# Performance work log

Measured on AMD Instinct MI355X. Metric: run time of the kernel, lower is better.

## Reference

```python
import jax, jax.numpy as jnp
import numpy as np

N, D_IN, D_HID, D_OUT, E = 8192, 1024, 4096, 1024, 8
N_ACTIVE = max(1, int(E * 0.625))  # 5
TEMP = float(np.e)               # temperature = np.e in source


def setup_inputs() -> dict:
    key = jax.random.key(0)
    ks = jax.random.split(key, 4)
    return {
        "x": jax.random.normal(ks[0], (N, D_IN), jnp.float32),
        "gate_w": jax.random.normal(ks[1], (D_IN, E), jnp.float32) * 0.02,
        "gate_b": jnp.zeros((E,), jnp.float32),
        "w1": jax.random.normal(ks[2], (E, D_IN, D_HID), jnp.float32) * 0.02,
        "b1": jnp.zeros((E, D_HID), jnp.float32),
        "w2": jax.random.normal(ks[3], (E, D_HID, D_OUT), jnp.float32) * 0.02,
        "b2": jnp.zeros((E, D_OUT), jnp.float32),
    }


def reference(x, gate_w, gate_b, w1, b1, w2, b2):
    # Gate: softmax over experts at temperature e, then top-k mask + renormalize
    scores = (x @ gate_w + gate_b) / TEMP                 # [N, E]
    probs = jax.nn.softmax(scores, axis=-1)               # [N, E]
    _, topk_idx = jax.lax.top_k(probs, N_ACTIVE)          # [N, k]
    mask = jax.nn.one_hot(topk_idx, E, dtype=probs.dtype).sum(axis=-2)  # [N, E]
    weights = probs * mask
    weights = weights / (weights.sum(axis=-1, keepdims=True) + 1e-8)
    # Dense all-experts FFN (dropout is eval-mode identity)
    h = jax.nn.relu(jnp.einsum('nd,edh->neh', x, w1) + b1)   # [N, E, d_hid]
    e_out = jnp.einsum('neh,eho->neo', h, w2) + b2           # [N, E, d_out]
    # Camp A (first E/2 experts) added, camp G subtracted: out = out_a - out_g
    sign = jnp.where(jnp.arange(E) < E // 2, 1.0, -1.0)      # [E]
    return jnp.einsum('ne,neo->no', weights * sign, e_out)   # [N, d_out]
```

## Files before the change

kernel.cpp:

```cpp
#include <hip/hip_runtime.h>
#include <hip/hip_bf16.h>
#include <cmath>


typedef _Float16 f16;
typedef _Float16 f16x8 __attribute__((ext_vector_type(8)));
typedef _Float16 f16x4 __attribute__((ext_vector_type(4)));
typedef float f32x4 __attribute__((ext_vector_type(4)));

#define NROWS 8192
#define DIN   1024
#define DHID  4096
#define DOUT  1024
#define NEXP  8

#define OFF_SGATE 0u
#define OFF_XH    262144u
#define OFF_W1T   17039360u
#define OFF_W2T   84148224u
#define OFF_HHS   151257088u
#define OFF_P1    218365952u
#define NEED_MID  251920384ull

__device__ __forceinline__ void gload_lds16(const void* gsrc, void* ldsdst) {
  __builtin_amdgcn_global_load_lds(
      (const __attribute__((address_space(1))) unsigned int*)gsrc,
      (__attribute__((address_space(3))) unsigned int*)ldsdst, 16, 0, 0);
}

__global__ void gate_kernel(const float* __restrict__ x,
                            const float* __restrict__ gw,
                            const float* __restrict__ gb,
                            float* __restrict__ sgate) {
  const int row = blockIdx.x * 4 + (threadIdx.x >> 6);
  const int l = threadIdx.x & 63;
  const float* xr = x + (size_t)row * DIN;
  float acc[8] = {0.f,0.f,0.f,0.f,0.f,0.f,0.f,0.f};
#pragma unroll
  for (int j = 0; j < 16; ++j) {
    const int k = l + 64 * j;
    const float xv = xr[k];
    const float4 g0 = *(const float4*)(gw + (size_t)k * 8);
    const float4 g1 = *(const float4*)(gw + (size_t)k * 8 + 4);
    acc[0] += xv * g0.x; acc[1] += xv * g0.y; acc[2] += xv * g0.z; acc[3] += xv * g0.w;
    acc[4] += xv * g1.x; acc[5] += xv * g1.y; acc[6] += xv * g1.z; acc[7] += xv * g1.w;
  }
#pragma unroll
  for (int off = 32; off > 0; off >>= 1) {
#pragma unroll
    for (int e = 0; e < 8; ++e) acc[e] += __shfl_xor(acc[e], off, 64);
  }
  if (l == 0) {
    const float invT = 0.36787944117144233f;
    float p[8]; float mx = -1e30f;
#pragma unroll
    for (int e = 0; e < 8; ++e) { p[e] = (acc[e] + gb[e]) * invT; mx = fmaxf(mx, p[e]); }
    float S = 0.f;
#pragma unroll
    for (int e = 0; e < 8; ++e) { p[e] = expf(p[e] - mx); S += p[e]; }
    const float inv = 1.0f / S;
#pragma unroll
    for (int e = 0; e < 8; ++e) p[e] *= inv;
    bool keep[8] = {true,true,true,true,true,true,true,true};
    for (int t = 0; t < 3; ++t) {
      float pmin = 1e30f; int mi = -1;
      for (int e = 0; e < 8; ++e)
        if (keep[e] && (p[e] < pmin || (p[e] == pmin && e > mi))) { pmin = p[e]; mi = e; }
      keep[mi] = false;
    }
    float wsum = 0.f;
#pragma unroll
    for (int e = 0; e < 8; ++e) if (keep[e]) wsum += p[e];
    const float rinv = 1.0f / (wsum + 1e-8f);
#pragma unroll
    for (int e = 0; e < 8; ++e) {
      const float wv = keep[e] ? p[e] * rinv : 0.0f;
      sgate[(size_t)row * 8 + e] = (e < 4) ? wv : -wv;
    }
  }
}

__global__ void cvt_x_kernel(const float* __restrict__ x, f16* __restrict__ xh) {
  const size_t i = ((size_t)blockIdx.x * blockDim.x + threadIdx.x) * 4;
  const float4 v = *(const float4*)(x + i);
  f16x4 o = { (f16)v.x, (f16)v.y, (f16)v.z, (f16)v.w };
  *(f16x4*)(xh + i) = o;
}

__global__ void transpose_cvt(const float* __restrict__ in, f16* __restrict__ out,
                              int R, int C) {
  __shared__ float tile[32][33];
  const int e = blockIdx.z;
  const float* ine = in + (size_t)e * R * C;
  f16* oute = out + (size_t)e * R * C;
  const int c0 = blockIdx.x * 32, r0 = blockIdx.y * 32;
  const int tx = threadIdx.x, ty = threadIdx.y;
#pragma unroll
  for (int i = 0; i < 4; ++i)
    tile[ty + i * 8][tx] = ine[(size_t)(r0 + ty + i * 8) * C + c0 + tx];
  __syncthreads();
#pragma unroll
  for (int i = 0; i < 4; ++i)
    oute[(size_t)(c0 + ty + i * 8) * R + r0 + tx] = (f16)tile[tx][ty + i * 8];
}

#define MFMAOP(a_, b_, c_) __builtin_amdgcn_mfma_f32_16x16x32_f16(a_, b_, c_, 0, 0, 0)

template <int EPI>
__global__ __launch_bounds__(512, 2) void gemm8p(
    const f16* __restrict__ A, int lda,
    const f16* __restrict__ B, int ldb, int nt,
    const float* __restrict__ bias,
    f16* __restrict__ outH, int ldc,
    float* outP0, float* outP1, int p1w,
    const float* __restrict__ sgate, int expert, int gx) {
  __shared__ alignas(16) f16 lA[4 * 8192];
  __shared__ alignas(16) f16 lB[4 * 8192];
  const int tid = threadIdx.x;
  const int l = tid & 63, w = tid >> 6;
  const int wr = w >> 2, wc = w & 3;

  const int nwg = gridDim.x, cpx = nwg >> 3;
  const int lg = ((int)blockIdx.x & 7) * cpx + ((int)blockIdx.x >> 3);

  int m0, n0;
  const f16* Aeff = A;
  const f16* Beff = B;
  float* P = nullptr;
  bool pw = false;
  if constexpr (EPI == 1) {
    m0 = (lg / gx) * 256; n0 = (lg % gx) * 256;
  } else {
    const int xx = lg >> 5, cc = lg & 31;
    const int kh = xx >> 2;
    n0 = (xx & 3) * 256;
    m0 = cc * 256;
    Aeff = A + kh * 2048;
    Beff = B + kh * 2048;
    P = kh ? outP1 : outP0;
    pw = (p1w != 0);
  }

  const int srow = tid >> 3;
  const int sxc = (tid & 7) ^ (srow & 7);
  const f16* pA = Aeff + (size_t)(m0 + srow) * lda + sxc * 8;
  const f16* pB = Beff + (size_t)(n0 + srow) * ldb + sxc * 8;
  f16* const dA = lA + w * 512;
  f16* const dB = lB + w * 512;

#define STG_A(slot, h, tk) do { \
    const f16* s_ = pA + (size_t)(h) * 128 * lda + (size_t)(tk) * 64; \
    gload_lds16(s_,            dA + (slot) * 8192); \
    gload_lds16(s_ + 64 * lda, dA + (slot) * 8192 + 4096); \
  } while (0)
#define STG_B(slot, h, tk) do { \
    const f16* s_ = pB + (size_t)(h) * 128 * ldb + (size_t)(tk) * 64; \
    gload_lds16(s_,            dB + (slot) * 8192); \
    gload_lds16(s_ + 64 * ldb, dB + (slot) * 8192 + 4096); \
  } while (0)

  const int cg = l >> 4, xr = l & 7;
  const int ok0 = ((cg ^ xr) << 4);
  const int ok1 = (((4 + cg) ^ xr) << 4);
  const char* const baA = (const char*)lA + (l & 15) * 128;
  const char* const baB = (const char*)lB + (wc & 1) * 8192 + (l & 15) * 128;

#define RDA(CA, f, o) (*(const f16x8*)(baA + ((CA) + wr) * 16384 + (f) * 2048 + (o)))
#define RDB(CB, g, o) (*(const f16x8*)(baB + ((CB) + (wc >> 1)) * 16384 + (g) * 2048 + (o)))
#define SYNC() do { __builtin_amdgcn_s_barrier(); \
    asm volatile("s_waitcnt lgkmcnt(0)" ::: "memory"); \
    __builtin_amdgcn_sched_barrier(0); } while (0)
#define ENDPH() do { __builtin_amdgcn_s_setprio(0); \
    __builtin_amdgcn_s_barrier(); } while (0)
#define VM6() do { asm volatile("s_waitcnt vmcnt(6)" ::: "memory"); \
    __builtin_amdgcn_sched_barrier(0); } while (0)
#define MM(f, g, ar, br) acc[f][g] = MFMAOP(ar, br, acc[f][g])

  f32x4 acc[8][4] = {};
  f16x8 aA0,aA1,aB0,aB1,aC0,aC1,aD0,aD1;
  f16x8 b00,b01,b10,b11,b20,b21,b30,b31;

#define TILEBODY(T, CA, CB, SB1, SB0n, SA0n, SA1n) do { \
     \
    aA0 = RDA(CA, 0, ok0); aA1 = RDA(CA, 0, ok1); \
    aB0 = RDA(CA, 1, ok0); aB1 = RDA(CA, 1, ok1); \
    aC0 = RDA(CA, 2, ok0); aC1 = RDA(CA, 2, ok1); \
    aD0 = RDA(CA, 3, ok0); aD1 = RDA(CA, 3, ok1); \
    b00 = RDB(CB, 0, ok0); b01 = RDB(CB, 0, ok1); \
    b10 = RDB(CB, 1, ok0); b11 = RDB(CB, 1, ok1); \
    if ((T) + 1 < nt) STG_B(SB1, 1, (T) + 1); \
    SYNC(); \
    __builtin_amdgcn_s_setprio(1); \
    MM(0,0,aA0,b00); MM(0,1,aA0,b10); MM(1,0,aB0,b00); MM(1,1,aB0,b10); \
    MM(2,0,aC0,b00); MM(2,1,aC0,b10); MM(3,0,aD0,b00); MM(3,1,aD0,b10); \
    MM(0,0,aA1,b01); MM(0,1,aA1,b11); MM(1,0,aB1,b01); MM(1,1,aB1,b11); \
    MM(2,0,aC1,b01); MM(2,1,aC1,b11); MM(3,0,aD1,b01); MM(3,1,aD1,b11); \
    ENDPH(); \
     \
    b20 = RDB(CB, 2, ok0); b21 = RDB(CB, 2, ok1); \
    b30 = RDB(CB, 3, ok0); b31 = RDB(CB, 3, ok1); \
    SYNC(); \
    __builtin_amdgcn_s_setprio(1); \
    MM(0,2,aA0,b20); MM(0,3,aA0,b30); MM(1,2,aB0,b20); MM(1,3,aB0,b30); \
    MM(2,2,aC0,b20); MM(2,3,aC0,b30); MM(3,2,aD0,b20); MM(3,3,aD0,b30); \
    MM(0,2,aA1,b21); MM(0,3,aA1,b31); MM(1,2,aB1,b21); MM(1,3,aB1,b31); \
    MM(2,2,aC1,b21); MM(2,3,aC1,b31); MM(3,2,aD1,b21); MM(3,3,aD1,b31); \
    ENDPH(); \
     \
    aA0 = RDA(CA, 4, ok0); aA1 = RDA(CA, 4, ok1); \
    aB0 = RDA(CA, 5, ok0); aB1 = RDA(CA, 5, ok1); \
    aC0 = RDA(CA, 6, ok0); aC1 = RDA(CA, 6, ok1); \
    aD0 = RDA(CA, 7, ok0); aD1 = RDA(CA, 7, ok1); \
    if ((T) + 2 < nt) STG_B(SB0n, 0, (T) + 2); \
    SYNC(); \
    __builtin_amdgcn_s_setprio(1); \
    MM(4,0,aA0,b00); MM(4,1,aA0,b10); MM(5,0,aB0,b00); MM(5,1,aB0,b10); \
    MM(6,0,aC0,b00); MM(6,1,aC0,b10); MM(7,0,aD0,b00); MM(7,1,aD0,b10); \
    MM(4,0,aA1,b01); MM(4,1,aA1,b11); MM(5,0,aB1,b01); MM(5,1,aB1,b11); \
    MM(6,0,aC1,b01); MM(6,1,aC1,b11); MM(7,0,aD1,b01); MM(7,1,aD1,b11); \
    ENDPH(); \
     \
    if ((T) + 2 < nt) { STG_A(SA0n, 0, (T) + 2); STG_A(SA1n, 1, (T) + 2); } \
    VM6(); \
    SYNC(); \
    __builtin_amdgcn_s_setprio(1); \
    MM(4,2,aA0,b20); MM(4,3,aA0,b30); MM(5,2,aB0,b20); MM(5,3,aB0,b30); \
    MM(6,2,aC0,b20); MM(6,3,aC0,b30); MM(7,2,aD0,b20); MM(7,3,aD0,b30); \
    MM(4,2,aA1,b21); MM(4,3,aA1,b31); MM(5,2,aB1,b21); MM(5,3,aB1,b31); \
    MM(6,2,aC1,b21); MM(6,3,aC1,b31); MM(7,2,aD1,b21); MM(7,3,aD1,b31); \
    ENDPH(); \
  } while (0)

  STG_A(0, 0, 0); STG_B(0, 0, 0); STG_A(1, 1, 0); STG_B(1, 1, 0);
  STG_A(2, 0, 1); STG_B(2, 0, 1); STG_A(3, 1, 1);
  asm volatile("s_waitcnt vmcnt(6)" ::: "memory");
  __builtin_amdgcn_s_barrier();

  for (int t = 0; t < nt; t += 2) {
    TILEBODY(t,     0, 0, 3, 0, 0, 1);
    TILEBODY(t + 1, 2, 2, 1, 2, 2, 3);
  }
  asm volatile("s_waitcnt vmcnt(0)" ::: "memory");

  if constexpr (EPI == 1) {
#pragma unroll
    for (int mi = 0; mi < 8; ++mi)
#pragma unroll
      for (int r = 0; r < 4; ++r) {
        const int row = m0 + wr * 128 + mi * 16 + (l >> 4) * 4 + r;
        const float sg = sgate[(size_t)row * 8 + expert];
#pragma unroll
        for (int ni = 0; ni < 4; ++ni) {
          const int col = n0 + wc * 64 + ni * 16 + (l & 15);
          const float v = acc[mi][ni][r] + bias[col];
          outH[(size_t)row * ldc + col] = (f16)(fmaxf(v, 0.0f) * sg);
        }
      }
  } else {
    float* const scr = (w < 4) ? (float*)lA + w * 4096
                               : (float*)lB + (w - 4) * 4096;
    const int hl = l >> 4, ll = l & 15;
#pragma unroll
    for (int p = 0; p < 2; ++p) {
#pragma unroll
      for (int mi4 = 0; mi4 < 4; ++mi4)
#pragma unroll
        for (int r = 0; r < 4; ++r) {
          const int rowl = mi4 * 16 + hl * 4 + r;
#pragma unroll
          for (int ni = 0; ni < 4; ++ni)
            scr[rowl * 64 + ni * 16 + ll] = acc[p * 4 + mi4][ni][r];
        }
#pragma unroll
      for (int i = 0; i < 16; ++i) {
        const int rowl = hl + i * 4;
        f32x4 v = *(const f32x4*)(scr + rowl * 64 + ll * 4);
        const int row = m0 + wr * 128 + p * 64 + rowl;
        const int col = n0 + wc * 64 + ll * 4;
        f32x4* gp = (f32x4*)(P + (size_t)row * 1024 + col);
        if (!pw) {
          const f32x4 g = *gp;
          v[0] += g[0]; v[1] += g[1]; v[2] += g[2]; v[3] += g[3];
        }
        *gp = v;
      }
    }
  }
#undef STG_A
#undef STG_B
#undef RDA
#undef RDB
#undef SYNC
#undef ENDPH
#undef VM6
#undef MM
#undef TILEBODY
}

template <bool WITHP>
__global__ void finalize_out(const float* p0,
                             const float* __restrict__ p1,
                             const float* __restrict__ sgate,
                             const float* __restrict__ b2,
                             float* out) {
  const int i = blockIdx.x * 256 + threadIdx.x;
  const int n = i >> 8, c4 = i & 255;
  float4 a = make_float4(0.f, 0.f, 0.f, 0.f);
  if constexpr (WITHP) {
    const float4 u = ((const float4*)p0)[i];
    const float4 v = ((const float4*)p1)[i];
    a.x = u.x + v.x; a.y = u.y + v.y; a.z = u.z + v.z; a.w = u.w + v.w;
  }
  const float* sg = sgate + (size_t)n * 8;
#pragma unroll
  for (int e = 0; e < 8; ++e) {
    const float s = sg[e];
    const float4 bv = ((const float4*)(b2 + (size_t)e * 1024))[c4];
    a.x += s * bv.x; a.y += s * bv.y; a.z += s * bv.z; a.w += s * bv.w;
  }
  ((float4*)out)[i] = a;
}

__global__ __launch_bounds__(512, 2) void gemm_acc(
    const f16* __restrict__ A, const f16* __restrict__ Bt,
    float* __restrict__ Out, int N, int K, int gx) {
  __shared__ alignas(16) f16 lA[3 * 256 * 64];
  __shared__ alignas(16) f16 lB[3 * 128 * 64];
  const int tid = threadIdx.x;
  const int l = tid & 63, w = tid >> 6;
  const int wr = w >> 1, wc = w & 1;
  const int nwg = gridDim.x, cpx = nwg >> 3;
  const int lg = ((int)blockIdx.x & 7) * cpx + ((int)blockIdx.x >> 3);
  const int bx = lg % gx, by = lg / gx;
  const int m0 = by * 256, n0 = bx * 128;

  const int srow = tid >> 3;
  const int scol = (((tid & 7) ^ (srow & 7)) << 3);
  const f16* Ab = A + ((size_t)m0 + srow) * K + scol;
  const f16* Bb = Bt + ((size_t)n0 + srow) * K + scol;
  f16* const dA = &lA[w * 512];
  f16* const dB = &lB[w * 512];

  int aoff[4][2], boff[4][2];
#pragma unroll
  for (int f = 0; f < 4; ++f) {
    const int ar = wr * 64 + f * 16 + (l & 15);
    const int br = wc * 64 + f * 16 + (l & 15);
#pragma unroll
    for (int ks = 0; ks < 2; ++ks) {
      const int cb = ks * 64 + ((l >> 4) << 4);
      aoff[f][ks] = ar * 64 + ((cb ^ ((ar & 7) << 4)) >> 1);
      boff[f][ks] = br * 64 + ((cb ^ ((br & 7) << 4)) >> 1);
    }
  }
  f32x4 acc[4][4] = {};
  f16x8 b[4][2];
  f16x8 aA, aB, aC, aD;
#define STAGE_A(bs, t) do { \
    const f16* s_ = Ab + (size_t)(t) * 64; \
    gload_lds16(s_,                   dA + (bs) * 16384); \
    gload_lds16(s_ + (size_t)64 * K,  dA + (bs) * 16384 + 4096); \
    gload_lds16(s_ + (size_t)128 * K, dA + (bs) * 16384 + 8192); \
    gload_lds16(s_ + (size_t)192 * K, dA + (bs) * 16384 + 12288); \
  } while (0)
#define STAGE_B(bs, t) do { \
    const f16* s_ = Bb + (size_t)(t) * 64; \
    gload_lds16(s_,                   dB + (bs) * 8192); \
    gload_lds16(s_ + (size_t)64 * K,  dB + (bs) * 8192 + 4096); \
  } while (0)
#define LOAD_B(bs) do { \
    b[0][0] = *(const f16x8*)&lB[(bs) * 8192 + boff[0][0]]; \
    b[0][1] = *(const f16x8*)&lB[(bs) * 8192 + boff[0][1]]; \
    b[1][0] = *(const f16x8*)&lB[(bs) * 8192 + boff[1][0]]; \
    b[1][1] = *(const f16x8*)&lB[(bs) * 8192 + boff[1][1]]; \
    b[2][0] = *(const f16x8*)&lB[(bs) * 8192 + boff[2][0]]; \
    b[2][1] = *(const f16x8*)&lB[(bs) * 8192 + boff[2][1]]; \
    b[3][0] = *(const f16x8*)&lB[(bs) * 8192 + boff[3][0]]; \
    b[3][1] = *(const f16x8*)&lB[(bs) * 8192 + boff[3][1]]; \
  } while (0)
#define LOAD_A4(bs, m0_, m1_) do { \
    aA = *(const f16x8*)&lA[(bs) * 16384 + aoff[m0_][0]]; \
    aB = *(const f16x8*)&lA[(bs) * 16384 + aoff[m0_][1]]; \
    aC = *(const f16x8*)&lA[(bs) * 16384 + aoff[m1_][0]]; \
    aD = *(const f16x8*)&lA[(bs) * 16384 + aoff[m1_][1]]; \
  } while (0)
#define CLUSTER(m0_, m1_) do { \
    __builtin_amdgcn_s_setprio(1); \
    acc[m0_][0] = MFMAOP(aA, b[0][0], acc[m0_][0]); \
    acc[m0_][1] = MFMAOP(aA, b[1][0], acc[m0_][1]); \
    acc[m0_][2] = MFMAOP(aA, b[2][0], acc[m0_][2]); \
    acc[m0_][3] = MFMAOP(aA, b[3][0], acc[m0_][3]); \
    acc[m1_][0] = MFMAOP(aC, b[0][0], acc[m1_][0]); \
    acc[m1_][1] = MFMAOP(aC, b[1][0], acc[m1_][1]); \
    acc[m1_][2] = MFMAOP(aC, b[2][0], acc[m1_][2]); \
    acc[m1_][3] = MFMAOP(aC, b[3][0], acc[m1_][3]); \
    acc[m0_][0] = MFMAOP(aB, b[0][1], acc[m0_][0]); \
    acc[m0_][1] = MFMAOP(aB, b[1][1], acc[m0_][1]); \
    acc[m0_][2] = MFMAOP(aB, b[2][1], acc[m0_][2]); \
    acc[m0_][3] = MFMAOP(aB, b[3][1], acc[m0_][3]); \
    acc[m1_][0] = MFMAOP(aD, b[0][1], acc[m1_][0]); \
    acc[m1_][1] = MFMAOP(aD, b[1][1], acc[m1_][1]); \
    acc[m1_][2] = MFMAOP(aD, b[2][1], acc[m1_][2]); \
    acc[m1_][3] = MFMAOP(aD, b[3][1], acc[m1_][3]); \
    __builtin_amdgcn_s_setprio(0); \
  } while (0)
#define BAR() asm volatile("s_barrier" ::: "memory")
#define VMC6() asm volatile("s_waitcnt vmcnt(6)" ::: "memory")
  const int niter = K >> 7, ntiles = K >> 6;
  STAGE_A(0, 0); STAGE_B(0, 0);
  STAGE_A(1, 1); STAGE_B(1, 1);
  VMC6();
  BAR();
  int bp = 0, bq = 1, brr = 2;
  int t2 = 2, t3 = 3;
  for (int i = 0; i < niter; ++i) {
    LOAD_B(bp); LOAD_A4(bp, 0, 1);
    STAGE_A(brr, t2);
    BAR(); CLUSTER(0, 1); BAR();
    LOAD_A4(bp, 2, 3);
    STAGE_B(brr, t2);
    VMC6(); BAR(); CLUSTER(2, 3); BAR();
    LOAD_B(bq); LOAD_A4(bq, 0, 1);
    STAGE_A(bp, t3);
    BAR(); CLUSTER(0, 1); BAR();
    LOAD_A4(bq, 2, 3);
    STAGE_B(bp, t3);
    VMC6(); BAR(); CLUSTER(2, 3); BAR();
    const int tmp = bp; bp = brr; brr = bq; bq = tmp;
    t2 += 2; if (t2 >= ntiles) t2 -= ntiles;
    t3 += 2; if (t3 >= ntiles) t3 -= ntiles;
  }
  asm volatile("s_waitcnt vmcnt(0)" ::: "memory");
#pragma unroll
  for (int mi = 0; mi < 4; ++mi)
#pragma unroll
    for (int r = 0; r < 4; ++r) {
      const int row = m0 + wr * 64 + mi * 16 + (l >> 4) * 4 + r;
#pragma unroll
      for (int ni = 0; ni < 4; ++ni) {
        const int col = n0 + wc * 64 + ni * 16 + (l & 15);
        Out[(size_t)row * N + col] += acc[mi][ni][r];
      }
    }
#undef STAGE_A
#undef STAGE_B
#undef LOAD_B
#undef LOAD_A4
#undef CLUSTER
#undef BAR
#undef VMC6
}

extern "C" void kernel_launch(void* const* d_in, const int* in_sizes, int n_in,
                              void* d_out, int out_size, void* d_ws, size_t ws_size,
                              hipStream_t stream) {
  const float* x  = (const float*)d_in[0];
  const float* gw = (const float*)d_in[1];
  const float* gb = (const float*)d_in[2];
  const float* w1 = (const float*)d_in[3];
  const float* b1 = (const float*)d_in[4];
  const float* w2 = (const float*)d_in[5];
  const float* b2 = (const float*)d_in[6];
  float* out = (float*)d_out;

  char* ws = (char*)d_ws;
  float* sgate = (float*)(ws + OFF_SGATE);
  f16* xh  = (f16*)(ws + OFF_XH);
  f16* w1t = (f16*)(ws + OFF_W1T);
  f16* w2t = (f16*)(ws + OFF_W2T);
  f16* hhs = (f16*)(ws + OFF_HHS);
  float* p1 = (float*)(ws + OFF_P1);

  const bool mid = (ws_size >= NEED_MID);

  gate_kernel<<<NROWS / 4, 256, 0, stream>>>(x, gw, gb, sgate);
  cvt_x_kernel<<<(NROWS * DIN) / (256 * 4), 256, 0, stream>>>(x, xh);
  transpose_cvt<<<dim3(DHID / 32, DIN / 32, NEXP), dim3(32, 8), 0, stream>>>(w1, w1t, DIN, DHID);
  transpose_cvt<<<dim3(DOUT / 32, DHID / 32, NEXP), dim3(32, 8), 0, stream>>>(w2, w2t, DHID, DOUT);

  if (mid) {
    for (int e = 0; e < NEXP; ++e) {
      gemm8p<1><<<512, 512, 0, stream>>>(
          xh, DIN, w1t + (size_t)e * DHID * DIN, DIN, DIN / 64,
          b1 + (size_t)e * DHID, hhs, DHID,
          nullptr, nullptr, 0, sgate, e, DHID / 256);
      gemm8p<2><<<256, 512, 0, stream>>>(
          hhs, DHID, w2t + (size_t)e * DOUT * DHID, DHID, 2048 / 64,
          nullptr, nullptr, 0, out, p1, (e == 0) ? 1 : 0, nullptr, 0, DOUT / 256);
    }
    finalize_out<true><<<(NROWS * DOUT) / (256 * 4), 256, 0, stream>>>(
        out, p1, sgate, b2, out);
  } else {
    finalize_out<false><<<(NROWS * DOUT) / (256 * 4), 256, 0, stream>>>(
        nullptr, nullptr, sgate, b2, out);
    for (int e = 0; e < NEXP; ++e) {
      gemm8p<1><<<512, 512, 0, stream>>>(
          xh, DIN, w1t + (size_t)e * DHID * DIN, DIN, DIN / 64,
          b1 + (size_t)e * DHID, hhs, DHID,
          nullptr, nullptr, 0, sgate, e, DHID / 256);
      gemm_acc<<<256, 512, 0, stream>>>(hhs, w2t + (size_t)e * DOUT * DHID,
                                        out, DOUT, DHID, DOUT / 128);
    }
  }
}
```

Before: 1.545 ms.

## Batch experts into grouped second GEMM with K=32 four-stage LDS pipeline

The GEMM tile loop changes from a K=64 step with three staged slots to a K=32 step with a four-slot ring and a new swizzle. The host now writes hidden activations for up to 8 experts side by side in a wider buffer, sized to fit the workspace. A single second GEMM then runs over the concatenated K of all experts in the group, so the fp32 partial sums are read and written once per group instead of once per expert. The fallback gemm_acc path is removed, and the workspace offsets and requirements change to match.

```diff
diff --git a/kernel.cpp b/kernel.cpp
--- a/kernel.cpp
+++ b/kernel.cpp
@@ -18,9 +18,12 @@
 #define OFF_XH    262144u
 #define OFF_W1T   17039360u
 #define OFF_W2T   84148224u
-#define OFF_HHS   151257088u
-#define OFF_P1    218365952u
-#define NEED_MID  251920384ull
+#define OFF_P1    151257088u
+#define OFF_HH    184811520u
+#define NEED_NE1  251920384ull
+#define NEED_NE2  319029248ull
+#define NEED_NE4  453246976ull
+#define NEED_NE8  721682432ull
 
 __device__ __forceinline__ void gload_lds16(const void* gsrc, void* ldsdst) {
   __builtin_amdgcn_global_load_lds(
@@ -110,6 +113,7 @@
 __global__ __launch_bounds__(512, 2) void gemm8p(
     const f16* __restrict__ A, int lda,
     const f16* __restrict__ B, int ldb, int nt,
+    long long khA, long long khB,
     const float* __restrict__ bias,
     f16* __restrict__ outH, int ldc,
     float* outP0, float* outP1, int p1w,
@@ -135,110 +139,100 @@
     const int kh = xx >> 2;
     n0 = (xx & 3) * 256;
     m0 = cc * 256;
-    Aeff = A + kh * 2048;
-    Beff = B + kh * 2048;
+    Aeff = A + (size_t)kh * (size_t)khA;
+    Beff = B + (size_t)kh * (size_t)khB;
     P = kh ? outP1 : outP0;
     pw = (p1w != 0);
   }
 
-  const int srow = tid >> 3;
-  const int sxc = (tid & 7) ^ (srow & 7);
+  const int srow = tid >> 2;
+  const int sxc = (tid & 3) ^ ((tid >> 3) & 3);
   const f16* pA = Aeff + (size_t)(m0 + srow) * lda + sxc * 8;
   const f16* pB = Beff + (size_t)(n0 + srow) * ldb + sxc * 8;
-  f16* const dA = lA + w * 512;
-  f16* const dB = lB + w * 512;
-
-#define STG_A(slot, h, tk) do { \
-    const f16* s_ = pA + (size_t)(h) * 128 * lda + (size_t)(tk) * 64; \
-    gload_lds16(s_,            dA + (slot) * 8192); \
-    gload_lds16(s_ + 64 * lda, dA + (slot) * 8192 + 4096); \
-  } while (0)
-#define STG_B(slot, h, tk) do { \
-    const f16* s_ = pB + (size_t)(h) * 128 * ldb + (size_t)(tk) * 64; \
-    gload_lds16(s_,            dB + (slot) * 8192); \
-    gload_lds16(s_ + 64 * ldb, dB + (slot) * 8192 + 4096); \
-  } while (0)
-
-  const int cg = l >> 4, xr = l & 7;
-  const int ok0 = ((cg ^ xr) << 4);
-  const int ok1 = (((4 + cg) ^ xr) << 4);
-  const char* const baA = (const char*)lA + (l & 15) * 128;
-  const char* const baB = (const char*)lB + (wc & 1) * 8192 + (l & 15) * 128;
-
-#define RDA(CA, f, o) (*(const f16x8*)(baA + ((CA) + wr) * 16384 + (f) * 2048 + (o)))
-#define RDB(CB, g, o) (*(const f16x8*)(baB + ((CB) + (wc >> 1)) * 16384 + (g) * 2048 + (o)))
+
+  auto BOFS = [&](int tk) -> size_t {
+    if constexpr (EPI == 1) return (size_t)tk * 32;
+    else return (size_t)(tk >> 7) * (size_t)(DOUT * DHID) +
+                (size_t)(tk & 127) * 32;
+  };
+
+#define STG_A(S, H, TK) \
+    gload_lds16(pA + (size_t)(H) * 128 * lda + (size_t)(TK) * 32, \
+                lA + (S) * 8192 + (H) * 4096 + w * 512)
+#define STG_B(S, H, TK) \
+    gload_lds16(pB + (size_t)(H) * 128 * ldb + BOFS(TK), \
+                lB + (S) * 8192 + (H) * 4096 + w * 512)
+
+  int aofs[8], bofs4[4];
+  {
+    const int cg = l >> 4;
+#pragma unroll
+    for (int f = 0; f < 8; ++f) {
+      const int r = wr * 128 + f * 16 + (l & 15);
+      aofs[f] = r * 64 + ((cg ^ ((r >> 1) & 3)) << 4);
+    }
+#pragma unroll
+    for (int g = 0; g < 4; ++g) {
+      const int r = wc * 64 + g * 16 + (l & 15);
+      bofs4[g] = r * 64 + ((cg ^ ((r >> 1) & 3)) << 4);
+    }
+  }
+#define RA(S, f) (*(const f16x8*)((const char*)lA + (S) * 16384 + aofs[f]))
+#define RB(S, g) (*(const f16x8*)((const char*)lB + (S) * 16384 + bofs4[g]))
+
 #define SYNC() do { __builtin_amdgcn_s_barrier(); \
     asm volatile("s_waitcnt lgkmcnt(0)" ::: "memory"); \
     __builtin_amdgcn_sched_barrier(0); } while (0)
 #define ENDPH() do { __builtin_amdgcn_s_setprio(0); \
     __builtin_amdgcn_s_barrier(); } while (0)
-#define VM6() do { asm volatile("s_waitcnt vmcnt(6)" ::: "memory"); \
+#define VM8() do { asm volatile("s_waitcnt vmcnt(8)" ::: "memory"); \
+    __builtin_amdgcn_sched_barrier(0); } while (0)
+#define VM4() do { asm volatile("s_waitcnt vmcnt(4)" ::: "memory"); \
+    __builtin_amdgcn_sched_barrier(0); } while (0)
+#define VM0() do { asm volatile("s_waitcnt vmcnt(0)" ::: "memory"); \
     __builtin_amdgcn_sched_barrier(0); } while (0)
 #define MM(f, g, ar, br) acc[f][g] = MFMAOP(ar, br, acc[f][g])
 
   f32x4 acc[8][4] = {};
-  f16x8 aA0,aA1,aB0,aB1,aC0,aC1,aD0,aD1;
-  f16x8 b00,b01,b10,b11,b20,b21,b30,b31;
-
-#define TILEBODY(T, CA, CB, SB1, SB0n, SA0n, SA1n) do { \
+  f16x8 fa0, fa1, fa2, fa3;
+  f16x8 fb0, fb1, fb2, fb3;
+
+#define BODY(T, S, S3) do { \
      \
-    aA0 = RDA(CA, 0, ok0); aA1 = RDA(CA, 0, ok1); \
-    aB0 = RDA(CA, 1, ok0); aB1 = RDA(CA, 1, ok1); \
-    aC0 = RDA(CA, 2, ok0); aC1 = RDA(CA, 2, ok1); \
-    aD0 = RDA(CA, 3, ok0); aD1 = RDA(CA, 3, ok1); \
-    b00 = RDB(CB, 0, ok0); b01 = RDB(CB, 0, ok1); \
-    b10 = RDB(CB, 1, ok0); b11 = RDB(CB, 1, ok1); \
-    if ((T) + 1 < nt) STG_B(SB1, 1, (T) + 1); \
+    fa0 = RA(S, 0); fa1 = RA(S, 1); fa2 = RA(S, 2); fa3 = RA(S, 3); \
+    fb0 = RB(S, 0); fb1 = RB(S, 1); fb2 = RB(S, 2); fb3 = RB(S, 3); \
+    if ((T) + 3 < nt) { STG_A(S3, 0, (T) + 3); STG_A(S3, 1, (T) + 3); } \
     SYNC(); \
     __builtin_amdgcn_s_setprio(1); \
-    MM(0,0,aA0,b00); MM(0,1,aA0,b10); MM(1,0,aB0,b00); MM(1,1,aB0,b10); \
-    MM(2,0,aC0,b00); MM(2,1,aC0,b10); MM(3,0,aD0,b00); MM(3,1,aD0,b10); \
-    MM(0,0,aA1,b01); MM(0,1,aA1,b11); MM(1,0,aB1,b01); MM(1,1,aB1,b11); \
-    MM(2,0,aC1,b01); MM(2,1,aC1,b11); MM(3,0,aD1,b01); MM(3,1,aD1,b11); \
+    MM(0,0,fa0,fb0); MM(0,1,fa0,fb1); MM(0,2,fa0,fb2); MM(0,3,fa0,fb3); \
+    MM(1,0,fa1,fb0); MM(1,1,fa1,fb1); MM(1,2,fa1,fb2); MM(1,3,fa1,fb3); \
+    MM(2,0,fa2,fb0); MM(2,1,fa2,fb1); MM(2,2,fa2,fb2); MM(2,3,fa2,fb3); \
+    MM(3,0,fa3,fb0); MM(3,1,fa3,fb1); MM(3,2,fa3,fb2); MM(3,3,fa3,fb3); \
     ENDPH(); \
      \
-    b20 = RDB(CB, 2, ok0); b21 = RDB(CB, 2, ok1); \
-    b30 = RDB(CB, 3, ok0); b31 = RDB(CB, 3, ok1); \
+    fa0 = RA(S, 4); fa1 = RA(S, 5); fa2 = RA(S, 6); fa3 = RA(S, 7); \
+    if ((T) + 3 < nt) { STG_B(S3, 0, (T) + 3); STG_B(S3, 1, (T) + 3); } \
+    if ((T) + 3 < nt) VM8(); else if ((T) + 2 < nt) VM4(); else VM0(); \
     SYNC(); \
     __builtin_amdgcn_s_setprio(1); \
-    MM(0,2,aA0,b20); MM(0,3,aA0,b30); MM(1,2,aB0,b20); MM(1,3,aB0,b30); \
-    MM(2,2,aC0,b20); MM(2,3,aC0,b30); MM(3,2,aD0,b20); MM(3,3,aD0,b30); \
-    MM(0,2,aA1,b21); MM(0,3,aA1,b31); MM(1,2,aB1,b21); MM(1,3,aB1,b31); \
-    MM(2,2,aC1,b21); MM(2,3,aC1,b31); MM(3,2,aD1,b21); MM(3,3,aD1,b31); \
-    ENDPH(); \
-     \
-    aA0 = RDA(CA, 4, ok0); aA1 = RDA(CA, 4, ok1); \
-    aB0 = RDA(CA, 5, ok0); aB1 = RDA(CA, 5, ok1); \
-    aC0 = RDA(CA, 6, ok0); aC1 = RDA(CA, 6, ok1); \
-    aD0 = RDA(CA, 7, ok0); aD1 = RDA(CA, 7, ok1); \
-    if ((T) + 2 < nt) STG_B(SB0n, 0, (T) + 2); \
-    SYNC(); \
-    __builtin_amdgcn_s_setprio(1); \
-    MM(4,0,aA0,b00); MM(4,1,aA0,b10); MM(5,0,aB0,b00); MM(5,1,aB0,b10); \
-    MM(6,0,aC0,b00); MM(6,1,aC0,b10); MM(7,0,aD0,b00); MM(7,1,aD0,b10); \
-    MM(4,0,aA1,b01); MM(4,1,aA1,b11); MM(5,0,aB1,b01); MM(5,1,aB1,b11); \
-    MM(6,0,aC1,b01); MM(6,1,aC1,b11); MM(7,0,aD1,b01); MM(7,1,aD1,b11); \
-    ENDPH(); \
-     \
-    if ((T) + 2 < nt) { STG_A(SA0n, 0, (T) + 2); STG_A(SA1n, 1, (T) + 2); } \
-    VM6(); \
-    SYNC(); \
-    __builtin_amdgcn_s_setprio(1); \
-    MM(4,2,aA0,b20); MM(4,3,aA0,b30); MM(5,2,aB0,b20); MM(5,3,aB0,b30); \
-    MM(6,2,aC0,b20); MM(6,3,aC0,b30); MM(7,2,aD0,b20); MM(7,3,aD0,b30); \
-    MM(4,2,aA1,b21); MM(4,3,aA1,b31); MM(5,2,aB1,b21); MM(5,3,aB1,b31); \
-    MM(6,2,aC1,b21); MM(6,3,aC1,b31); MM(7,2,aD1,b21); MM(7,3,aD1,b31); \
+    MM(4,0,fa0,fb0); MM(4,1,fa0,fb1); MM(4,2,fa0,fb2); MM(4,3,fa0,fb3); \
+    MM(5,0,fa1,fb0); MM(5,1,fa1,fb1); MM(5,2,fa1,fb2); MM(5,3,fa1,fb3); \
+    MM(6,0,fa2,fb0); MM(6,1,fa2,fb1); MM(6,2,fa2,fb2); MM(6,3,fa2,fb3); \
+    MM(7,0,fa3,fb0); MM(7,1,fa3,fb1); MM(7,2,fa3,fb2); MM(7,3,fa3,fb3); \
     ENDPH(); \
   } while (0)
 
-  STG_A(0, 0, 0); STG_B(0, 0, 0); STG_A(1, 1, 0); STG_B(1, 1, 0);
-  STG_A(2, 0, 1); STG_B(2, 0, 1); STG_A(3, 1, 1);
-  asm volatile("s_waitcnt vmcnt(6)" ::: "memory");
+  STG_A(0, 0, 0); STG_A(0, 1, 0); STG_B(0, 0, 0); STG_B(0, 1, 0);
+  STG_A(1, 0, 1); STG_A(1, 1, 1); STG_B(1, 0, 1); STG_B(1, 1, 1);
+  STG_A(2, 0, 2); STG_A(2, 1, 2); STG_B(2, 0, 2); STG_B(2, 1, 2);
+  VM8();
   __builtin_amdgcn_s_barrier();
 
-  for (int t = 0; t < nt; t += 2) {
-    TILEBODY(t,     0, 0, 3, 0, 0, 1);
-    TILEBODY(t + 1, 2, 2, 1, 2, 2, 3);
+  for (int T = 0; T < nt; T += 4) {
+    BODY(T + 0, 0, 3);
+    BODY(T + 1, 1, 0);
+    BODY(T + 2, 2, 1);
+    BODY(T + 3, 3, 2);
   }
   asm volatile("s_waitcnt vmcnt(0)" ::: "memory");
 
@@ -288,13 +282,15 @@
   }
 #undef STG_A
 #undef STG_B
-#undef RDA
-#undef RDB
+#undef RA
+#undef RB
 #undef SYNC
 #undef ENDPH
-#undef VM6
+#undef VM8
+#undef VM4
+#undef VM0
 #undef MM
-#undef TILEBODY
+#undef BODY
 }
 
 template <bool WITHP>
@@ -321,136 +317,6 @@
   ((float4*)out)[i] = a;
 }
 
-__global__ __launch_bounds__(512, 2) void gemm_acc(
-    const f16* __restrict__ A, const f16* __restrict__ Bt,
-    float* __restrict__ Out, int N, int K, int gx) {
-  __shared__ alignas(16) f16 lA[3 * 256 * 64];
-  __shared__ alignas(16) f16 lB[3 * 128 * 64];
-  const int tid = threadIdx.x;
-  const int l = tid & 63, w = tid >> 6;
-  const int wr = w >> 1, wc = w & 1;
-  const int nwg = gridDim.x, cpx = nwg >> 3;
-  const int lg = ((int)blockIdx.x & 7) * cpx + ((int)blockIdx.x >> 3);
-  const int bx = lg % gx, by = lg / gx;
-  const int m0 = by * 256, n0 = bx * 128;
-
-  const int srow = tid >> 3;
-  const int scol = (((tid & 7) ^ (srow & 7)) << 3);
-  const f16* Ab = A + ((size_t)m0 + srow) * K + scol;
-  const f16* Bb = Bt + ((size_t)n0 + srow) * K + scol;
-  f16* const dA = &lA[w * 512];
-  f16* const dB = &lB[w * 512];
-
-  int aoff[4][2], boff[4][2];
-#pragma unroll
-  for (int f = 0; f < 4; ++f) {
-    const int ar = wr * 64 + f * 16 + (l & 15);
-    const int br = wc * 64 + f * 16 + (l & 15);
-#pragma unroll
-    for (int ks = 0; ks < 2; ++ks) {
-      const int cb = ks * 64 + ((l >> 4) << 4);
-      aoff[f][ks] = ar * 64 + ((cb ^ ((ar & 7) << 4)) >> 1);
-      boff[f][ks] = br * 64 + ((cb ^ ((br & 7) << 4)) >> 1);
-    }
-  }
-  f32x4 acc[4][4] = {};
-  f16x8 b[4][2];
-  f16x8 aA, aB, aC, aD;
-#define STAGE_A(bs, t) do { \
-    const f16* s_ = Ab + (size_t)(t) * 64; \
-    gload_lds16(s_,                   dA + (bs) * 16384); \
-    gload_lds16(s_ + (size_t)64 * K,  dA + (bs) * 16384 + 4096); \
-    gload_lds16(s_ + (size_t)128 * K, dA + (bs) * 16384 + 8192); \
-    gload_lds16(s_ + (size_t)192 * K, dA + (bs) * 16384 + 12288); \
-  } while (0)
-#define STAGE_B(bs, t) do { \
-    const f16* s_ = Bb + (size_t)(t) * 64; \
-    gload_lds16(s_,                   dB + (bs) * 8192); \
-    gload_lds16(s_ + (size_t)64 * K,  dB + (bs) * 8192 + 4096); \
-  } while (0)
-#define LOAD_B(bs) do { \
-    b[0][0] = *(const f16x8*)&lB[(bs) * 8192 + boff[0][0]]; \
-    b[0][1] = *(const f16x8*)&lB[(bs) * 8192 + boff[0][1]]; \
-    b[1][0] = *(const f16x8*)&lB[(bs) * 8192 + boff[1][0]]; \
-    b[1][1] = *(const f16x8*)&lB[(bs) * 8192 + boff[1][1]]; \
-    b[2][0] = *(const f16x8*)&lB[(bs) * 8192 + boff[2][0]]; \
-    b[2][1] = *(const f16x8*)&lB[(bs) * 8192 + boff[2][1]]; \
-    b[3][0] = *(const f16x8*)&lB[(bs) * 8192 + boff[3][0]]; \
-    b[3][1] = *(const f16x8*)&lB[(bs) * 8192 + boff[3][1]]; \
-  } while (0)
-#define LOAD_A4(bs, m0_, m1_) do { \
-    aA = *(const f16x8*)&lA[(bs) * 16384 + aoff[m0_][0]]; \
-    aB = *(const f16x8*)&lA[(bs) * 16384 + aoff[m0_][1]]; \
-    aC = *(const f16x8*)&lA[(bs) * 16384 + aoff[m1_][0]]; \
-    aD = *(const f16x8*)&lA[(bs) * 16384 + aoff[m1_][1]]; \
-  } while (0)
-#define CLUSTER(m0_, m1_) do { \
-    __builtin_amdgcn_s_setprio(1); \
-    acc[m0_][0] = MFMAOP(aA, b[0][0], acc[m0_][0]); \
-    acc[m0_][1] = MFMAOP(aA, b[1][0], acc[m0_][1]); \
-    acc[m0_][2] = MFMAOP(aA, b[2][0], acc[m0_][2]); \
-    acc[m0_][3] = MFMAOP(aA, b[3][0], acc[m0_][3]); \
-    acc[m1_][0] = MFMAOP(aC, b[0][0], acc[m1_][0]); \
-    acc[m1_][1] = MFMAOP(aC, b[1][0], acc[m1_][1]); \
-    acc[m1_][2] = MFMAOP(aC, b[2][0], acc[m1_][2]); \
-    acc[m1_][3] = MFMAOP(aC, b[3][0], acc[m1_][3]); \
-    acc[m0_][0] = MFMAOP(aB, b[0][1], acc[m0_][0]); \
-    acc[m0_][1] = MFMAOP(aB, b[1][1], acc[m0_][1]); \
-    acc[m0_][2] = MFMAOP(aB, b[2][1], acc[m0_][2]); \
-    acc[m0_][3] = MFMAOP(aB, b[3][1], acc[m0_][3]); \
-    acc[m1_][0] = MFMAOP(aD, b[0][1], acc[m1_][0]); \
-    acc[m1_][1] = MFMAOP(aD, b[1][1], acc[m1_][1]); \
-    acc[m1_][2] = MFMAOP(aD, b[2][1], acc[m1_][2]); \
-    acc[m1_][3] = MFMAOP(aD, b[3][1], acc[m1_][3]); \
-    __builtin_amdgcn_s_setprio(0); \
-  } while (0)
-#define BAR() asm volatile("s_barrier" ::: "memory")
-#define VMC6() asm volatile("s_waitcnt vmcnt(6)" ::: "memory")
-  const int niter = K >> 7, ntiles = K >> 6;
-  STAGE_A(0, 0); STAGE_B(0, 0);
-  STAGE_A(1, 1); STAGE_B(1, 1);
-  VMC6();
-  BAR();
-  int bp = 0, bq = 1, brr = 2;
-  int t2 = 2, t3 = 3;
-  for (int i = 0; i < niter; ++i) {
-    LOAD_B(bp); LOAD_A4(bp, 0, 1);
-    STAGE_A(brr, t2);
-    BAR(); CLUSTER(0, 1); BAR();
-    LOAD_A4(bp, 2, 3);
-    STAGE_B(brr, t2);
-    VMC6(); BAR(); CLUSTER(2, 3); BAR();
-    LOAD_B(bq); LOAD_A4(bq, 0, 1);
-    STAGE_A(bp, t3);
-    BAR(); CLUSTER(0, 1); BAR();
-    LOAD_A4(bq, 2, 3);
-    STAGE_B(bp, t3);
-    VMC6(); BAR(); CLUSTER(2, 3); BAR();
-    const int tmp = bp; bp = brr; brr = bq; bq = tmp;
-    t2 += 2; if (t2 >= ntiles) t2 -= ntiles;
-    t3 += 2; if (t3 >= ntiles) t3 -= ntiles;
-  }
-  asm volatile("s_waitcnt vmcnt(0)" ::: "memory");
-#pragma unroll
-  for (int mi = 0; mi < 4; ++mi)
-#pragma unroll
-    for (int r = 0; r < 4; ++r) {
-      const int row = m0 + wr * 64 + mi * 16 + (l >> 4) * 4 + r;
-#pragma unroll
-      for (int ni = 0; ni < 4; ++ni) {
-        const int col = n0 + wc * 64 + ni * 16 + (l & 15);
-        Out[(size_t)row * N + col] += acc[mi][ni][r];
-      }
-    }
-#undef STAGE_A
-#undef STAGE_B
-#undef LOAD_B
-#undef LOAD_A4
-#undef CLUSTER
-#undef BAR
-#undef VMC6
-}
-
 extern "C" void kernel_launch(void* const* d_in, const int* in_sizes, int n_in,
                               void* d_out, int out_size, void* d_ws, size_t ws_size,
                               hipStream_t stream) {
@@ -468,38 +334,34 @@
   f16* xh  = (f16*)(ws + OFF_XH);
   f16* w1t = (f16*)(ws + OFF_W1T);
   f16* w2t = (f16*)(ws + OFF_W2T);
-  f16* hhs = (f16*)(ws + OFF_HHS);
   float* p1 = (float*)(ws + OFF_P1);
-
-  const bool mid = (ws_size >= NEED_MID);
+  f16* hh  = (f16*)(ws + OFF_HH);
+
+  const int NE = (ws_size >= NEED_NE8) ? 8 :
+                 (ws_size >= NEED_NE4) ? 4 :
+                 (ws_size >= NEED_NE2) ? 2 : 1;
 
   gate_kernel<<<NROWS / 4, 256, 0, stream>>>(x, gw, gb, sgate);
   cvt_x_kernel<<<(NROWS * DIN) / (256 * 4), 256, 0, stream>>>(x, xh);
   transpose_cvt<<<dim3(DHID / 32, DIN / 32, NEXP), dim3(32, 8), 0, stream>>>(w1, w1t, DIN, DHID);
   transpose_cvt<<<dim3(DOUT / 32, DHID / 32, NEXP), dim3(32, 8), 0, stream>>>(w2, w2t, DHID, DOUT);
 
-  if (mid) {
-    for (int e = 0; e < NEXP; ++e) {
+  const int ngrp = NEXP / NE;
+  const long long khB = (NE == 1) ? 2048LL : (long long)(NE / 2) * DOUT * DHID;
+  for (int g = 0; g < ngrp; ++g) {
+    for (int ei = 0; ei < NE; ++ei) {
+      const int e = g * NE + ei;
       gemm8p<1><<<512, 512, 0, stream>>>(
-          xh, DIN, w1t + (size_t)e * DHID * DIN, DIN, DIN / 64,
-          b1 + (size_t)e * DHID, hhs, DHID,
+          xh, DIN, w1t + (size_t)e * DHID * DIN, DIN, DIN / 32,
+          0, 0,
+          b1 + (size_t)e * DHID, hh + (size_t)ei * DHID, NE * DHID,
           nullptr, nullptr, 0, sgate, e, DHID / 256);
-      gemm8p<2><<<256, 512, 0, stream>>>(
-          hhs, DHID, w2t + (size_t)e * DOUT * DHID, DHID, 2048 / 64,
-          nullptr, nullptr, 0, out, p1, (e == 0) ? 1 : 0, nullptr, 0, DOUT / 256);
-    }
-    finalize_out<true><<<(NROWS * DOUT) / (256 * 4), 256, 0, stream>>>(
-        out, p1, sgate, b2, out);
-  } else {
-    finalize_out<false><<<(NROWS * DOUT) / (256 * 4), 256, 0, stream>>>(
-        nullptr, nullptr, sgate, b2, out);
-    for (int e = 0; e < NEXP; ++e) {
-      gemm8p<1><<<512, 512, 0, stream>>>(
-          xh, DIN, w1t + (size_t)e * DHID * DIN, DIN, DIN / 64,
-          b1 + (size_t)e * DHID, hhs, DHID,
-          nullptr, nullptr, 0, sgate, e, DHID / 256);
-      gemm_acc<<<256, 512, 0, stream>>>(hhs, w2t + (size_t)e * DOUT * DHID,
-                                        out, DOUT, DHID, DOUT / 128);
-    }
-  }
-}
+    }
+    gemm8p<2><<<256, 512, 0, stream>>>(
+        hh, NE * DHID, w2t + (size_t)g * NE * DOUT * DHID, DHID, NE * 64,
+        (long long)NE * 2048, khB,
+        nullptr, nullptr, 0, out, p1, (g == 0) ? 1 : 0, nullptr, 0, 0);
+  }
+  finalize_out<true><<<(NROWS * DOUT) / (256 * 4), 256, 0, stream>>>(
+      out, p1, sgate, b2, out);
+}
```

New measurement: 1.633 ms. +5.7%, slower.
